# Optimization experiments

Hardware: AMD Instinct MI355X
Metric: run time of the kernel (lower is better)

## Reference

```python
import jax, jax.numpy as jnp
import numpy as np

B, S, D, H = 2, 2048, 1024, 16
HD = D // H          # 64
HALF = HD // 2       # 32
EPS = 1e-6           # RMSNorm eps (module default eps=1e-6)


def setup_inputs() -> dict:
    key = jax.random.key(0)
    ks = jax.random.split(key, 6)
    x = jax.random.normal(ks[0], (B, S, D), jnp.float32)
    scale = 1.0 / np.sqrt(D)
    Wq = jax.random.normal(ks[1], (D, D), jnp.float32) * scale
    Wk = jax.random.normal(ks[2], (D, D), jnp.float32) * scale
    Wv = jax.random.normal(ks[3], (D, D), jnp.float32) * scale
    Wo = jax.random.normal(ks[4], (D, D), jnp.float32) * scale
    bq = jnp.zeros((D,), jnp.float32)
    bk = jnp.zeros((D,), jnp.float32)
    bv = jnp.zeros((D,), jnp.float32)
    bo = jnp.zeros((D,), jnp.float32)
    gq = jnp.ones((D,), jnp.float32)   # norm_q weight
    gk = jnp.ones((D,), jnp.float32)   # norm_k weight
    # Standard RoPE angles: pos * 10000^(-2i/head_dim); freqs = exp(i*ang)
    pos = jnp.arange(S, dtype=jnp.float32)
    inv_freq = 1.0 / (10000.0 ** (jnp.arange(0, HD, 2, dtype=jnp.float32) / HD))
    ang = pos[:, None] * inv_freq[None, :]          # (S, HALF)
    return dict(x=x, Wq=Wq, bq=bq, Wk=Wk, bk=bk, Wv=Wv, bv=bv, Wo=Wo, bo=bo,
                gq=gq, gk=gk, freqs_cos=jnp.cos(ang), freqs_sin=jnp.sin(ang))


def _rmsnorm(x, g):
    # x * rsqrt(mean(x^2) + eps) * g, computed in fp32 as in the torch module
    return x * jax.lax.rsqrt(jnp.mean(x * x, axis=-1, keepdims=True) + EPS) * g


def _rope(x, cos, sin):
    # x: (B,S,D) packed heads; rotate consecutive (even,odd) pairs per head.
    xr = x.reshape(B, S, H, HALF, 2)
    x0, x1 = xr[..., 0], xr[..., 1]
    c = cos[None, :, None, :]  # (1,S,1,HALF)
    s = sin[None, :, None, :]
    o0 = x0 * c - x1 * s
    o1 = x0 * s + x1 * c
    return jnp.stack([o0, o1], axis=-1).reshape(B, S, D)


def reference(x, Wq, bq, Wk, bk, Wv, bv, Wo, bo, gq, gk, freqs_cos, freqs_sin):
    q = _rmsnorm(x @ Wq.T + bq, gq)
    k = _rmsnorm(x @ Wk.T + bk, gk)
    v = x @ Wv.T + bv
    q = _rope(q, freqs_cos, freqs_sin)
    k = _rope(k, freqs_cos, freqs_sin)
    # SDPA (non-causal, as F.scaled_dot_product_attention default call)
    qh = q.reshape(B, S, H, HD)
    kh = k.reshape(B, S, H, HD)
    vh = v.reshape(B, S, H, HD)
    scores = jnp.einsum('bqhd,bkhd->bhqk', qh, kh) / np.sqrt(HD)
    attn = jax.nn.softmax(scores, axis=-1)
    out = jnp.einsum('bhqk,bkhd->bqhd', attn, vh).reshape(B, S, D)
    return out @ Wo.T + bo
```

## Files before the change

kernel.cpp:

```cpp
#include <hip/hip_runtime.h>

typedef unsigned short u16;
typedef unsigned int u32;
typedef u16 u16x4 __attribute__((ext_vector_type(4)));
typedef u16 u16x8 __attribute__((ext_vector_type(8)));
typedef u32 u32x4 __attribute__((ext_vector_type(4)));
typedef float f32x4 __attribute__((ext_vector_type(4)));
typedef float f32x16 __attribute__((ext_vector_type(16)));
typedef __bf16 bf16x2 __attribute__((ext_vector_type(2)));
typedef __bf16 bf16x8 __attribute__((ext_vector_type(8)));

#define GLOAD16(gp, lp)                                             \
  __builtin_amdgcn_global_load_lds(                                 \
      (const __attribute__((address_space(1))) void*)(gp),          \
      (__attribute__((address_space(3))) void*)(lp), 16, 0, 0)

__device__ __forceinline__ u16 f2bf(float f) {
  unsigned int u = __builtin_bit_cast(unsigned int, f);
  u += 0x7FFFu + ((u >> 16) & 1u);
  return (u16)(u >> 16);
}
__device__ __forceinline__ float bf2f(u16 h) {
  return __builtin_bit_cast(float, (u32)h << 16);
}

__global__ __launch_bounds__(256) void f2ball_kernel(const float* __restrict__ x,
    const float* __restrict__ w0, const float* __restrict__ w1,
    const float* __restrict__ w2, const float* __restrict__ w3,
    u16* __restrict__ xb, u16* __restrict__ wb) {
  int g = blockIdx.x * 256 + threadIdx.x;
  const float* s;
  u16* d;
  size_t off;
  if (g < 1048576) {
    s = x; d = xb; off = (size_t)g * 4;
  } else {
    int wi = g - 1048576;
    int sel = wi >> 18;
    int r = wi & 262143;
    s = (sel == 0) ? w0 : ((sel == 1) ? w1 : ((sel == 2) ? w2 : w3));
    d = wb + (size_t)sel * 1048576;
    off = (size_t)r * 4;
  }
  f32x4 v = *(const f32x4*)(s + off);
  u16x4 o;
  o[0] = f2bf(v[0]); o[1] = f2bf(v[1]); o[2] = f2bf(v[2]); o[3] = f2bf(v[3]);
  *(u16x4*)(d + off) = o;
}

__device__ __forceinline__ void gemm_core(const u16* __restrict__ A,
                                          const u16* __restrict__ W,
                                          int bm0, int bn0,
                                          u16* ldsA, u16* ldsB,
                                          f32x4 acc[4][4]) {
  const int tid = threadIdx.x;
  const int l = tid & 63;
  const int lr = l & 15, lk = l >> 4;
  const int w = tid >> 6;
  const int wr = w >> 1, wc = w & 1;
  const int srow = tid >> 2, sko = (tid & 3) << 3;
  auto stage = [&](int kt, int buf) {
#pragma unroll
    for (int it = 0; it < 2; ++it) {
      int row = it * 64 + srow;
      GLOAD16(A + (size_t)(bm0 + row) * 1024 + kt * 32 + sko,
              ldsA + buf * 4096 + (it * 256 + tid) * 8);
      GLOAD16(W + (size_t)(bn0 + row) * 1024 + kt * 32 + sko,
              ldsB + buf * 4096 + (it * 256 + tid) * 8);
    }
  };
  stage(0, 0);
  stage(1, 1);
  int cur = 0, nx2 = 2;
  for (int kt = 0; kt < 32; ++kt) {
    if (kt < 31) asm volatile("s_waitcnt vmcnt(4)" ::: "memory");
    else         asm volatile("s_waitcnt vmcnt(0)" ::: "memory");
    __builtin_amdgcn_s_barrier();
    __builtin_amdgcn_sched_barrier(0);
    if (kt + 2 < 32) stage(kt + 2, nx2);
    const u16* lA = ldsA + cur * 4096;
    const u16* lB = ldsB + cur * 4096;
    bf16x8 af[4], bfr[4];
#pragma unroll
    for (int m = 0; m < 4; ++m)
      af[m] = *(const bf16x8*)(lA + (wr * 64 + m * 16 + lr) * 32 + lk * 8);
#pragma unroll
    for (int n = 0; n < 4; ++n)
      bfr[n] = *(const bf16x8*)(lB + (wc * 64 + n * 16 + lr) * 32 + lk * 8);
#pragma unroll
    for (int m = 0; m < 4; ++m)
#pragma unroll
      for (int n = 0; n < 4; ++n)
        acc[m][n] = __builtin_amdgcn_mfma_f32_16x16x32_bf16(af[m], bfr[n], acc[m][n], 0, 0, 0);
    cur = (cur == 2) ? 0 : cur + 1;
    nx2 = (nx2 == 2) ? 0 : nx2 + 1;
  }
}

__global__ __launch_bounds__(256) void qkv_gemm(const u16* __restrict__ xb,
    const u16* __restrict__ wq, const u16* __restrict__ wk, const u16* __restrict__ wv,
    const float* __restrict__ bq, const float* __restrict__ bk, const float* __restrict__ bv,
    u16* __restrict__ Qb, u16* __restrict__ Kb, u16* __restrict__ Vf) {
  __shared__ u16 ldsA[3 * 4096];
  __shared__ u16 ldsB[3 * 4096];
  const int z = blockIdx.z;
  const u16* W = (z == 0) ? wq : ((z == 1) ? wk : wv);
  const float* bias = (z == 0) ? bq : ((z == 1) ? bk : bv);
  const int bm0 = blockIdx.x * 128, bn0 = blockIdx.y * 128;
  const f32x4 zf = {0.f, 0.f, 0.f, 0.f};
  f32x4 acc[4][4];
#pragma unroll
  for (int m = 0; m < 4; ++m)
#pragma unroll
    for (int n = 0; n < 4; ++n) acc[m][n] = zf;
  gemm_core(xb, W, bm0, bn0, ldsA, ldsB, acc);
  const int tid = threadIdx.x, l = tid & 63, lr = l & 15, lk = l >> 4;
  const int w = tid >> 6, wr = w >> 1, wc = w & 1;
  float bcol[4];
#pragma unroll
  for (int n = 0; n < 4; ++n) bcol[n] = bias[bn0 + wc * 64 + n * 16 + lr];
  if (z < 2) {
    u16* outp = z ? Kb : Qb;
#pragma unroll
    for (int m = 0; m < 4; ++m)
#pragma unroll
      for (int n = 0; n < 4; ++n)
#pragma unroll
        for (int r = 0; r < 4; ++r) {
          int row = bm0 + wr * 64 + m * 16 + lk * 4 + r;
          int col = bn0 + wc * 64 + n * 16 + lr;
          outp[(size_t)row * 1024 + col] = f2bf(acc[m][n][r] + bcol[n]);
        }
  } else {
#pragma unroll
    for (int m = 0; m < 4; ++m)
#pragma unroll
      for (int n = 0; n < 4; ++n) {
        int row = bm0 + wr * 64 + m * 16 + lk * 4;
        int col = bn0 + wc * 64 + n * 16 + lr;
        int b = row >> 11, sf = row & 2047, hh = col >> 6, hd = col & 63;
        int t = sf >> 6, kin = sf & 63;
        int ks = kin >> 4, hiv = (kin >> 3) & 1, j0 = kin & 7;
        int vhalf = hd >> 5, lq = hd & 31;
        u16x4 o;
#pragma unroll
        for (int r = 0; r < 4; ++r) o[r] = f2bf(acc[m][n][r] + bcol[n]);
        size_t addr = (size_t)(b * 16 + hh) * 131072 +
                      (size_t)(((t * 4 + ks) * 2 + vhalf)) * 512 +
                      ((hiv << 5) + lq) * 8 + j0;
        *(u16x4*)(Vf + addr) = o;
      }
  }
}

__global__ __launch_bounds__(256) void proj_gemm(const u16* __restrict__ ctx,
    const u16* __restrict__ wo, const float* __restrict__ bo, float* __restrict__ out) {
  __shared__ u16 ldsA[3 * 4096];
  __shared__ u16 ldsB[3 * 4096];
  const int bm0 = blockIdx.x * 128, bn0 = blockIdx.y * 128;
  const f32x4 zf = {0.f, 0.f, 0.f, 0.f};
  f32x4 acc[4][4];
#pragma unroll
  for (int m = 0; m < 4; ++m)
#pragma unroll
    for (int n = 0; n < 4; ++n) acc[m][n] = zf;
  gemm_core(ctx, wo, bm0, bn0, ldsA, ldsB, acc);
  const int tid = threadIdx.x, l = tid & 63, lr = l & 15, lk = l >> 4;
  const int w = tid >> 6, wr = w >> 1, wc = w & 1;
  float bcol[4];
#pragma unroll
  for (int n = 0; n < 4; ++n) bcol[n] = bo[bn0 + wc * 64 + n * 16 + lr];
#pragma unroll
  for (int m = 0; m < 4; ++m)
#pragma unroll
    for (int n = 0; n < 4; ++n)
#pragma unroll
      for (int r = 0; r < 4; ++r) {
        int row = bm0 + wr * 64 + m * 16 + lk * 4 + r;
        int col = bn0 + wc * 64 + n * 16 + lr;
        out[(size_t)row * 1024 + col] = acc[m][n][r] + bcol[n];
      }
}

__global__ __launch_bounds__(256) void rmsrope(const u16* __restrict__ Qb,
    const u16* __restrict__ Kb, const float* __restrict__ gq, const float* __restrict__ gk,
    const float* __restrict__ fc, const float* __restrict__ fs,
    u16* __restrict__ Qf, u16* __restrict__ Kf) {
  const int row = blockIdx.x;
  const int which = blockIdx.y;
  const u16* src = (which ? Kb : Qb) + (size_t)row * 1024;
  const float* g = which ? gk : gq;
  const int t = threadIdx.x;
  u16x4 raw = *(const u16x4*)(src + t * 4);
  float v0 = bf2f(raw[0]), v1 = bf2f(raw[1]), v2 = bf2f(raw[2]), v3 = bf2f(raw[3]);
  float ss = v0 * v0 + v1 * v1 + v2 * v2 + v3 * v3;
#pragma unroll
  for (int mm = 1; mm < 64; mm <<= 1) ss += __shfl_xor(ss, mm);
  __shared__ float red[4];
  if ((t & 63) == 0) red[t >> 6] = ss;
  __syncthreads();
  float rstd = rsqrtf((red[0] + red[1] + red[2] + red[3]) * (1.0f / 1024.0f) + 1e-6f);
  if (!which) rstd *= 0.18033688011112042f;
  int d = t * 4, hh = d >> 6, dh = d & 63, p = dh >> 1;
  int s = row & 2047, b = row >> 11;
  float c0 = fc[(s << 5) + p], s0 = fs[(s << 5) + p];
  float c1 = fc[(s << 5) + p + 1], s1 = fs[(s << 5) + p + 1];
  float x0 = v0 * rstd * g[d];
  float x1 = v1 * rstd * g[d + 1];
  float x2 = v2 * rstd * g[d + 2];
  float x3 = v3 * rstd * g[d + 3];
  u16x4 o;
  o[0] = f2bf(x0 * c0 - x1 * s0);
  o[1] = f2bf(x0 * s0 + x1 * c0);
  o[2] = f2bf(x2 * c1 - x3 * s1);
  o[3] = f2bf(x2 * s1 + x3 * c1);
  const size_t base = (size_t)(b * 16 + hh) * 131072;
  const int hs = dh >> 4, hi = (dh >> 3) & 1, j0 = dh & 7;
  size_t addr;
  if (!which) {
    addr = base + (size_t)((s >> 5) * 4 + hs) * 512 + ((hi << 5) + (s & 31)) * 8 + j0;
  } else {
    addr = base + (size_t)(((s >> 6) * 4 + hs) * 2 + ((s >> 5) & 1)) * 512 +
           ((hi << 5) + (s & 31)) * 8 + j0;
  }
  *(u16x4*)((which ? Kf : Qf) + addr) = o;
}

__global__ __launch_bounds__(256) void attn_kernel(const u16* __restrict__ Qf,
    const u16* __restrict__ Kf, const u16* __restrict__ Vf, u16* __restrict__ ctx) {
  __shared__ u16 Kbuf[3][4096];
  const int tid = threadIdx.x;
  const int w = tid >> 6, l = tid & 63;
  const int lq = l & 31, hi = l >> 5;
  const bool hiB = (hi != 0);
  const int id = blockIdx.x;
  const int qt = (id >> 3) & 15;
  const int hb = (id & 7) | ((id >> 7) << 3);
  const int h = hb & 15, b = hb >> 4;
  const int bh = b * 16 + h;
  const u16* Qp = Qf + (size_t)bh * 131072;
  const u16* Kp = Kf + (size_t)bh * 131072;
  const u16* Vp = Vf + (size_t)bh * 131072;
  bf16x8 qf[4];
#pragma unroll
  for (int hs = 0; hs < 4; ++hs)
    qf[hs] = *(const bf16x8*)(Qp + (size_t)((qt * 4 + w) * 4 + hs) * 512 + l * 8);

  auto stageK = [&](int t, int buf) {
    GLOAD16(Kp + (size_t)t * 4096 + tid * 8, &Kbuf[buf][tid * 8]);
    GLOAD16(Kp + (size_t)t * 4096 + 2048 + tid * 8, &Kbuf[buf][2048 + tid * 8]);
  };
  auto ldV = [&](int t, bf16x8* vr) {
#pragma unroll
    for (int i = 0; i < 8; ++i)
      vr[i] = *(const bf16x8*)(Vp + ((size_t)t * 8 + i) * 512 + l * 8);
  };

  const f32x16 z16 = {0,0,0,0, 0,0,0,0, 0,0,0,0, 0,0,0,0};
  f32x16 O0 = z16, O1 = z16;
  float lsum = 0.f;

  auto qk_lds = [&](const u16* Kb_, f32x16& s0, f32x16& s1) {
    s0 = z16; s1 = z16;
    __builtin_amdgcn_s_setprio(1);
#pragma unroll
    for (int hs = 0; hs < 4; ++hs) {
      bf16x8 k0 = *(const bf16x8*)(Kb_ + (hs * 2 + 0) * 512 + l * 8);
      bf16x8 k1 = *(const bf16x8*)(Kb_ + (hs * 2 + 1) * 512 + l * 8);
      s0 = __builtin_amdgcn_mfma_f32_32x32x16_bf16(k0, qf[hs], s0, 0, 0, 0);
      s1 = __builtin_amdgcn_mfma_f32_32x32x16_bf16(k1, qf[hs], s1, 0, 0, 0);
    }
    __builtin_amdgcn_s_setprio(0);
  };

  auto sm_pv = [&](const bf16x8* vr, f32x16& sc0, f32x16& sc1) {
    float rs = 0.f;
    u32 pk0[8], pk1[8];
#pragma unroll
    for (int m = 0; m < 8; ++m) {
      float a0 = __builtin_amdgcn_exp2f(sc0[2 * m]);
      float a1 = __builtin_amdgcn_exp2f(sc0[2 * m + 1]);
      float c0 = __builtin_amdgcn_exp2f(sc1[2 * m]);
      float c1 = __builtin_amdgcn_exp2f(sc1[2 * m + 1]);
      rs += (a0 + a1) + (c0 + c1);
      bf16x2 pA; pA[0] = (__bf16)a0; pA[1] = (__bf16)a1;
      bf16x2 pC; pC[0] = (__bf16)c0; pC[1] = (__bf16)c1;
      pk0[m] = __builtin_bit_cast(u32, pA);
      pk1[m] = __builtin_bit_cast(u32, pC);
    }
    rs += __shfl_xor(rs, 32);
    lsum += rs;
    auto xchg = [&](u32 X, u32 Y, u32& wlo, u32& whi) {
      u32 s1v = hiB ? X : Y;
      u32 r = (u32)__shfl_xor((int)s1v, 32);
      wlo = hiB ? r : X;
      whi = hiB ? Y : r;
    };
    bf16x8 pb[4];
    {
      u32 w0, w1, w2, w3;
      xchg(pk0[0], pk0[2], w0, w2);
      xchg(pk0[1], pk0[3], w1, w3);
      u32x4 pw = {w0, w1, w2, w3};
      pb[0] = __builtin_bit_cast(bf16x8, pw);
      xchg(pk0[4], pk0[6], w0, w2);
      xchg(pk0[5], pk0[7], w1, w3);
      u32x4 pw1 = {w0, w1, w2, w3};
      pb[1] = __builtin_bit_cast(bf16x8, pw1);
      xchg(pk1[0], pk1[2], w0, w2);
      xchg(pk1[1], pk1[3], w1, w3);
      u32x4 pw2 = {w0, w1, w2, w3};
      pb[2] = __builtin_bit_cast(bf16x8, pw2);
      xchg(pk1[4], pk1[6], w0, w2);
      xchg(pk1[5], pk1[7], w1, w3);
      u32x4 pw3 = {w0, w1, w2, w3};
      pb[3] = __builtin_bit_cast(bf16x8, pw3);
    }
    __builtin_amdgcn_s_setprio(1);
#pragma unroll
    for (int ks = 0; ks < 4; ++ks) {
      O0 = __builtin_amdgcn_mfma_f32_32x32x16_bf16(vr[ks * 2 + 0], pb[ks], O0, 0, 0, 0);
      O1 = __builtin_amdgcn_mfma_f32_32x32x16_bf16(vr[ks * 2 + 1], pb[ks], O1, 0, 0, 0);
    }
    __builtin_amdgcn_s_setprio(0);
  };

  bf16x8 vV[8];
  f32x16 scX0, scX1;
  stageK(0, 0);
  stageK(1, 1);
  int cur = 0, nx2 = 2;
#pragma unroll 1
  for (int t = 0; t < 32; ++t) {
    if (t < 31) asm volatile("s_waitcnt vmcnt(2)" ::: "memory");
    else        asm volatile("s_waitcnt vmcnt(0)" ::: "memory");
    __builtin_amdgcn_s_barrier();
    __builtin_amdgcn_sched_barrier(0);
    ldV(t, vV);
    if (t + 2 < 32) stageK(t + 2, nx2);
    qk_lds(&Kbuf[cur][0], scX0, scX1);
    sm_pv(vV, scX0, scX1);
    cur = (cur == 2) ? 0 : cur + 1;
    nx2 = (nx2 == 2) ? 0 : nx2 + 1;
  }
  float inv = 1.0f / lsum;
  const int q0 = qt * 128 + w * 32;
  const size_t rowoff = ((size_t)(b * 2048 + q0 + lq)) * 1024 + h * 64;
#pragma unroll
  for (int g = 0; g < 4; ++g) {
    u16x4 oa, ob;
#pragma unroll
    for (int rr = 0; rr < 4; ++rr) {
      oa[rr] = f2bf(O0[4 * g + rr] * inv);
      ob[rr] = f2bf(O1[4 * g + rr] * inv);
    }
    *(u16x4*)(ctx + rowoff + 8 * g + 4 * hi) = oa;
    *(u16x4*)(ctx + rowoff + 32 + 8 * g + 4 * hi) = ob;
  }
}

extern "C" void kernel_launch(void* const* d_in, const int* in_sizes, int n_in,
                              void* d_out, int out_size, void* d_ws, size_t ws_size,
                              hipStream_t stream) {
  (void)in_sizes; (void)n_in; (void)out_size; (void)ws_size;
  const float* x  = (const float*)d_in[0];
  const float* Wq = (const float*)d_in[1];
  const float* bq = (const float*)d_in[2];
  const float* Wk = (const float*)d_in[3];
  const float* bk = (const float*)d_in[4];
  const float* Wv = (const float*)d_in[5];
  const float* bv = (const float*)d_in[6];
  const float* Wo = (const float*)d_in[7];
  const float* bo = (const float*)d_in[8];
  const float* gq = (const float*)d_in[9];
  const float* gk = (const float*)d_in[10];
  const float* fc = (const float*)d_in[11];
  const float* fs = (const float*)d_in[12];
  float* out = (float*)d_out;
  char* ws = (char*)d_ws;
  u16*  xb  = (u16*)(ws + 0);
  u16*  wqb = (u16*)(ws + 8388608);
  u16*  wkb = (u16*)(ws + 10485760);
  u16*  wvb = (u16*)(ws + 12582912);
  u16*  wob = (u16*)(ws + 14680064);
  u16*  Qfb = (u16*)(ws + 16777216);
  u16*  Kfb = (u16*)(ws + 25165824);
  u16*  Qfr = (u16*)(ws + 33554432);
  u16*  Kfr = (u16*)(ws + 41943040);
  u16*  Vfr = (u16*)(ws + 50331648);
  u16*  ctx = (u16*)(ws + 58720256);

  f2ball_kernel<<<8192, 256, 0, stream>>>(x, Wq, Wk, Wv, Wo, xb, wqb);
  qkv_gemm<<<dim3(32, 8, 3), 256, 0, stream>>>(xb, wqb, wkb, wvb, bq, bk, bv, Qfb, Kfb, Vfr);
  rmsrope<<<dim3(4096, 2), 256, 0, stream>>>(Qfb, Kfb, gq, gk, fc, fs, Qfr, Kfr);
  attn_kernel<<<512, 256, 0, stream>>>(Qfr, Kfr, Vfr, ctx);
  proj_gemm<<<dim3(32, 8), 256, 0, stream>>>(ctx, wob, bo, out);
}
```

Baseline: 141.2 us.

## Software-pipeline QK^T one tile ahead of softmax and PV in attention loop

The attention main loop is unrolled by two. Each step issues the QK^T MFMAs for the next K tile before running exp/softmax and the PV MFMAs on the current tile's scores. Three rotating LDS pointers replace the index arithmetic, and a third K tile is prefetched up front. The per-row exp sum becomes a tree reduction instead of a serial chain. The explicit vmcnt waits inside the loop are gone, so it relies on compiler-inserted waits before the barriers, which risks reading LDS before the asynchronous K loads land. It also raises register pressure with a second pair of score accumulators.

```diff
diff --git a/kernel.cpp b/kernel.cpp
--- a/kernel.cpp
+++ b/kernel.cpp
@@ -246,9 +246,9 @@
   for (int hs = 0; hs < 4; ++hs)
     qf[hs] = *(const bf16x8*)(Qp + (size_t)((qt * 4 + w) * 4 + hs) * 512 + l * 8);
 
-  auto stageK = [&](int t, int buf) {
-    GLOAD16(Kp + (size_t)t * 4096 + tid * 8, &Kbuf[buf][tid * 8]);
-    GLOAD16(Kp + (size_t)t * 4096 + 2048 + tid * 8, &Kbuf[buf][2048 + tid * 8]);
+  auto stageK = [&](int t, u16* dst) {
+    GLOAD16(Kp + (size_t)t * 4096 + tid * 8, dst + tid * 8);
+    GLOAD16(Kp + (size_t)t * 4096 + 2048 + tid * 8, dst + 2048 + tid * 8);
   };
   auto ldV = [&](int t, bf16x8* vr) {
 #pragma unroll
@@ -274,20 +274,22 @@
   };
 
   auto sm_pv = [&](const bf16x8* vr, f32x16& sc0, f32x16& sc1) {
-    float rs = 0.f;
     u32 pk0[8], pk1[8];
+    float tm[8];
 #pragma unroll
     for (int m = 0; m < 8; ++m) {
       float a0 = __builtin_amdgcn_exp2f(sc0[2 * m]);
       float a1 = __builtin_amdgcn_exp2f(sc0[2 * m + 1]);
       float c0 = __builtin_amdgcn_exp2f(sc1[2 * m]);
       float c1 = __builtin_amdgcn_exp2f(sc1[2 * m + 1]);
-      rs += (a0 + a1) + (c0 + c1);
+      tm[m] = (a0 + a1) + (c0 + c1);
       bf16x2 pA; pA[0] = (__bf16)a0; pA[1] = (__bf16)a1;
       bf16x2 pC; pC[0] = (__bf16)c0; pC[1] = (__bf16)c1;
       pk0[m] = __builtin_bit_cast(u32, pA);
       pk1[m] = __builtin_bit_cast(u32, pC);
     }
+    float rs = ((tm[0] + tm[1]) + (tm[2] + tm[3])) +
+               ((tm[4] + tm[5]) + (tm[6] + tm[7]));
     rs += __shfl_xor(rs, 32);
     lsum += rs;
     auto xchg = [&](u32 X, u32 Y, u32& wlo, u32& whi) {
@@ -326,22 +328,37 @@
   };
 
   bf16x8 vV[8];
-  f32x16 scX0, scX1;
-  stageK(0, 0);
-  stageK(1, 1);
-  int cur = 0, nx2 = 2;
+  f32x16 scA0, scA1, scB0, scB1;
+  u16* pA = &Kbuf[0][0];
+  u16* pB = &Kbuf[1][0];
+  u16* pC = &Kbuf[2][0];
+  stageK(0, pA);
+  stageK(1, pB);
+  stageK(2, pC);
+  asm volatile("s_waitcnt vmcnt(2)" ::: "memory");
+  __builtin_amdgcn_s_barrier();
+  __builtin_amdgcn_sched_barrier(0);
+  qk_lds(pA, scA0, scA1);
 #pragma unroll 1
-  for (int t = 0; t < 32; ++t) {
-    if (t < 31) asm volatile("s_waitcnt vmcnt(2)" ::: "memory");
-    else        asm volatile("s_waitcnt vmcnt(0)" ::: "memory");
-    __builtin_amdgcn_s_barrier();
-    __builtin_amdgcn_sched_barrier(0);
-    ldV(t, vV);
-    if (t + 2 < 32) stageK(t + 2, nx2);
-    qk_lds(&Kbuf[cur][0], scX0, scX1);
-    sm_pv(vV, scX0, scX1);
-    cur = (cur == 2) ? 0 : cur + 1;
-    nx2 = (nx2 == 2) ? 0 : nx2 + 1;
+  for (int dt = 0; dt < 16; ++dt) {
+    const int t = dt * 2;
+    {
+      __builtin_amdgcn_s_barrier();
+      __builtin_amdgcn_sched_barrier(0);
+      ldV(t, vV);
+      if (t + 3 < 32) stageK(t + 3, pA);
+      qk_lds(pB, scB0, scB1);
+      sm_pv(vV, scA0, scA1);
+    }
+    {
+      __builtin_amdgcn_s_barrier();
+      __builtin_amdgcn_sched_barrier(0);
+      ldV(t + 1, vV);
+      if (t + 4 < 32) stageK(t + 4, pB);
+      if (t + 2 < 32) qk_lds(pC, scA0, scA1);
+      sm_pv(vV, scB0, scB1);
+    }
+    u16* tmp = pA; pA = pC; pC = pB; pB = tmp;
   }
   float inv = 1.0f / lsum;
   const int q0 = qt * 128 + w * 32;
```

After: 134.8 us. 1.05x faster.
